# Optimization experiments

Hardware: AMD Instinct MI355X
Metric: run time of the kernel (lower is better)

Reference implementation:

```python
import jax, jax.numpy as jnp
import numpy as np

DMODEL = 1024
N_EXPERTS = 16
EXPERT_SIZE = 256
K = 4


def setup_inputs() -> dict:
    key = jax.random.key(0)
    k1, k2, k3, k4 = jax.random.split(key, 4)
    std_sel = 1.0 / np.sqrt(DMODEL)
    std_val = 1.0 / np.sqrt(N_EXPERTS * EXPERT_SIZE)
    return {
        "x": jax.random.normal(k1, (4, 2048, DMODEL), dtype=jnp.float32),
        "expert_sel": jax.random.normal(k2, (N_EXPERTS, DMODEL), dtype=jnp.float32) * std_sel,
        "keys": jax.random.normal(k3, (N_EXPERTS, DMODEL, EXPERT_SIZE), dtype=jnp.float32) * std_sel,
        "values": jax.random.normal(k4, (N_EXPERTS, EXPERT_SIZE, DMODEL), dtype=jnp.float32) * std_val,
        "route_scale": jnp.ones((1,), dtype=jnp.float32),
    }


def reference(x, expert_sel, keys, values, route_scale):
    # Routing: sigmoid gating, top-k selection (eval mode: no dropout/bias balancing)
    sel_logits = jnp.einsum("btd,ed->bte", x, expert_sel)  # [B,T,E]
    sel_probs = jax.nn.sigmoid(sel_logits)
    _, sel_index = jax.lax.top_k(sel_probs, K)  # [B,T,K]
    sel_val = jnp.take_along_axis(sel_probs, sel_index, axis=-1)  # [B,T,K]
    sel_val = sel_val / jnp.clip(sel_val.sum(-1, keepdims=True), 1e-9)
    sel_val = sel_val * route_scale  # route_scale shape [1] broadcasts
    # Dense all-expert FFN (as in original), then gather top-k and combine
    scores_all = jax.nn.relu(jnp.einsum("btd,edh->bteh", x, keys))  # [B,T,E,H]
    values_all = jnp.einsum("bteh,ehv->btev", scores_all, values)   # [B,T,E,V]
    sel_idx_exp = sel_index[..., None]  # [B,T,K,1]
    selected = jnp.take_along_axis(values_all, sel_idx_exp, axis=2)  # [B,T,K,V]
    out = (selected * sel_val[..., None]).sum(axis=2)  # [B,T,V]
    return out
```

## Files before the change

### kernel.cpp

```cpp
#include <hip/hip_runtime.h>
#include <math.h>


constexpr int NTOK = 8192;
constexpr int DM   = 1024;
constexpr int NE   = 16;
constexpr int EH   = 256;
constexpr int TK   = 4;
constexpr int CAP  = 8192;
constexpr int BM   = 64;

typedef __attribute__((ext_vector_type(8))) short short8;
typedef __attribute__((ext_vector_type(4))) float f32x4;

#define MFMA16(a, b, c) __builtin_amdgcn_mfma_f32_16x16x32_bf16(a, b, c, 0, 0, 0)
#define VMCNT(n) asm volatile("s_waitcnt vmcnt(" #n ")" ::: "memory")
#define SBAR     __builtin_amdgcn_s_barrier()
#define SCHED0   __builtin_amdgcn_sched_barrier(0)

__device__ __forceinline__ void gload_lds16(const void* g, void* l) {
    __builtin_amdgcn_global_load_lds(
        (const __attribute__((address_space(1))) void*)g,
        (__attribute__((address_space(3))) void*)l, 16, 0, 0);
}

__device__ __forceinline__ unsigned short f2bf(float f) {
    union { float f; unsigned int u; } x; x.f = f;
    unsigned int r = x.u + 0x7fffu + ((x.u >> 16) & 1u);
    return (unsigned short)(r >> 16);
}
__device__ __forceinline__ float bf2f(unsigned short b) {
    union { unsigned int u; float f; } x; x.u = ((unsigned int)b) << 16;
    return x.f;
}

__global__ __launch_bounds__(256) void route_conv_kernel(
    const float* __restrict__ x, const float* __restrict__ esel,
    const float* __restrict__ rscale,
    unsigned short* __restrict__ xb,
    int4* __restrict__ sel4, float* __restrict__ wtk)
{
    __shared__ float Es[NE * DM];
    int tid = threadIdx.x;

    {
        const float4* src = (const float4*)esel;
        float4* dst = (float4*)Es;
        #pragma unroll
        for (int j = 0; j < 16; ++j) dst[tid + j * 256] = src[tid + j * 256];
    }
    __syncthreads();

    int t    = blockIdx.x * 8 + (tid >> 5);
    int l32  = tid & 31;

    float acc[NE];
    #pragma unroll
    for (int e = 0; e < NE; ++e) acc[e] = 0.f;

    const float4* x4 = (const float4*)(x + (size_t)t * DM);
    const float4* E4 = (const float4*)Es;
    #pragma unroll
    for (int i4 = 0; i4 < 8; ++i4) {
        int d4 = i4 * 32 + l32;
        float4 xv = x4[d4];
        ushort4 cb = { f2bf(xv.x), f2bf(xv.y), f2bf(xv.z), f2bf(xv.w) };
        *(ushort4*)(xb + (size_t)t * DM + d4 * 4) = cb;
        #pragma unroll
        for (int e = 0; e < NE; ++e) {
            float4 wv = E4[e * 256 + d4];
            acc[e] = fmaf(xv.x, wv.x, acc[e]);
            acc[e] = fmaf(xv.y, wv.y, acc[e]);
            acc[e] = fmaf(xv.z, wv.z, acc[e]);
            acc[e] = fmaf(xv.w, wv.w, acc[e]);
        }
    }

    #pragma unroll
    for (int off = 16; off; off >>= 1)
        #pragma unroll
        for (int e = 0; e < NE; ++e)
            acc[e] += __shfl_xor(acc[e], off, 32);

    if (l32 == 0) {
        float p[NE];
        #pragma unroll
        for (int e = 0; e < NE; ++e) p[e] = 1.0f / (1.0f + expf(-acc[e]));

        int   sel_e[TK];
        float sel_p[TK];
        float sum = 0.f;
        #pragma unroll
        for (int k = 0; k < TK; ++k) {
            float best = -INFINITY; int be = NE;
            #pragma unroll
            for (int e = 0; e < NE; ++e) {
                bool take = p[e] > best;
                best = take ? p[e] : best;
                be   = take ? e    : be;
            }
            sel_e[k] = be; sel_p[k] = best; sum += best;
            #pragma unroll
            for (int e = 0; e < NE; ++e) p[e] = (e == be) ? -INFINITY : p[e];
        }

        float wsc = rscale[0] / fmaxf(sum, 1e-9f);
        int4 s = { sel_e[0], sel_e[1], sel_e[2], sel_e[3] };
        sel4[t] = s;
        float4 wv = { sel_p[0] * wsc, sel_p[1] * wsc,
                      sel_p[2] * wsc, sel_p[3] * wsc };
        *(float4*)(wtk + t * TK) = wv;
    }
}

__global__ __launch_bounds__(1024) void compact_kernel(
    const int4* __restrict__ sel4, int* __restrict__ counts,
    int* __restrict__ lpk)
{
    __shared__ int wsum[16];
    int e    = blockIdx.x;
    int tid  = threadIdx.x;
    int w    = tid >> 6;
    int lane = tid & 63;

    int base = 0;
    for (int c = 0; c < NTOK; c += 1024) {
        int t = c + tid;
        int4 s = sel4[t];
        int k = -1;
        if      (s.x == e) k = 0;
        else if (s.y == e) k = 1;
        else if (s.z == e) k = 2;
        else if (s.w == e) k = 3;
        unsigned long long m = __ballot(k >= 0);
        int rank = __popcll(m & ((1ull << lane) - 1ull));
        if (lane == 63) wsum[w] = __popcll(m);
        __syncthreads();
        int prefix = 0, total = 0;
        #pragma unroll
        for (int i = 0; i < 16; ++i) {
            int v = wsum[i];
            prefix += (i < w) ? v : 0;
            total  += v;
        }
        if (k >= 0) lpk[e * CAP + base + prefix + rank] = t * TK + k;
        base += total;
        __syncthreads();
    }
    if (tid == 0) counts[e] = base;
}

__global__ __launch_bounds__(256) void transF_kernel(
    const float* __restrict__ in, unsigned short* __restrict__ outp, int R, int C)
{
    __shared__ float T[32][33];
    int e = blockIdx.z;
    int r0 = blockIdx.y * 32, c0 = blockIdx.x * 32;
    int ri = threadIdx.x >> 3, cq = threadIdx.x & 7;
    float4 v = *(const float4*)(in + ((size_t)e * R + r0 + ri) * C + c0 + cq * 4);
    T[ri][cq * 4 + 0] = v.x; T[ri][cq * 4 + 1] = v.y;
    T[ri][cq * 4 + 2] = v.z; T[ri][cq * 4 + 3] = v.w;
    __syncthreads();
    int ci = threadIdx.x >> 3, rq = threadIdx.x & 7;
    int row = c0 + ci;
    int kb  = r0 + rq * 4;
    int nk32 = R >> 5;
    size_t chunk = (size_t)e * (C >> 4) * nk32 + (size_t)(row >> 4) * nk32 + (kb >> 5);
    size_t off = chunk * 512 +
                 (size_t)(((((kb >> 3) & 3) * 16 + (row & 15)) * 8) + (kb & 7));
    ushort4 o = { f2bf(T[rq * 4 + 0][ci]), f2bf(T[rq * 4 + 1][ci]),
                  f2bf(T[rq * 4 + 2][ci]), f2bf(T[rq * 4 + 3][ci]) };
    *(ushort4*)(outp + off) = o;
}

template<int USE_SCRATCH>
__global__ __launch_bounds__(256) void ffn_kernel(
    const unsigned short* __restrict__ xb,
    const unsigned short* __restrict__ ktbF,
    const unsigned short* __restrict__ vtbF,
    const int* __restrict__ counts, const int* __restrict__ lpk,
    const float* __restrict__ wtk,
    unsigned short* __restrict__ scratch,
    float* __restrict__ out)
{
    __shared__ __align__(16) char L[12288 + 32768 + 768];
    char* const Xb = L;
    char* const Ss = L + 12288;
    int*   stok = (int*)(L + 45056);
    int*   spk  = (int*)(L + 45056 + 256);
    float* sw   = (float*)(L + 45056 + 512);

    int tid  = threadIdx.x;
    int lane = tid & 63;
    int w    = tid >> 6;
    int lm   = lane & 15;
    int q    = lane >> 4;
    int lane8 = lane * 8;

    int xp = blockIdx.x & 7;
    int j0 = blockIdx.x >> 3;
    int e0 = xp * 2;
    int c0 = counts[e0], c1 = counts[e0 + 1];
    int n0 = (c0 + BM - 1) >> 6;
    int ntot = n0 + ((c1 + BM - 1) >> 6);

    for (int jt = j0; jt < ntot; jt += 64) {
        int e, t0, cnt;
        if (jt < n0) { e = e0;     t0 = jt << 6;        cnt = c0; }
        else         { e = e0 + 1; t0 = (jt - n0) << 6; cnt = c1; }

        if (tid < BM) {
            int s = t0 + tid;
            if (s < cnt) {
                int pk = lpk[e * CAP + s];
                stok[tid] = pk >> 2; spk[tid] = pk; sw[tid] = wtk[pk];
            } else {
                stok[tid] = 0; spk[tid] = USE_SCRATCH ? (NTOK * TK) : 0; sw[tid] = 0.f;
            }
        }
        __syncthreads();

        int rowX = tid >> 2;
        int cb   = ((tid & 3) * 16) ^ (((rowX >> 1) & 3) << 4);
        const unsigned short* srcX = xb + (size_t)stok[rowX] * DM + (cb >> 1);
        const unsigned short* kfe  = ktbF + (size_t)e * 262144;
        const unsigned short* vfe  = vtbF + (size_t)e * 262144;
        int w4  = w * 4;
        int w16 = w * 16;

        auto stageX = [&](int n) {
            if (n < 32)
                gload_lds16(srcX + n * 32, Xb + (n % 3) * 4096 + tid * 16);
        };
        auto loadK = [&](short8 (&kr)[4], int n) {
            if (n < 32) {
                #pragma unroll
                for (int ni = 0; ni < 4; ++ni)
                    kr[ni] = *(const short8*)(kfe + (((w4 + ni) * 32 + n) << 9) + lane8);
            }
        };

        f32x4 zero = {0.f, 0.f, 0.f, 0.f};
        f32x4 acc[4][4];
        #pragma unroll
        for (int mi = 0; mi < 4; ++mi)
            #pragma unroll
            for (int ni = 0; ni < 4; ++ni) acc[mi][ni] = zero;

        short8 krA[4], krB[4];

        stageX(0); stageX(1); loadK(krA, 0);
        SCHED0;
        loadK(krB, 1);
        SCHED0;

        auto step1 = [&](int n, short8 (&kr)[4]) {
            if (n == 0)       { VMCNT(4); }
            else if (n == 31) { VMCNT(0); }
            else              { VMCNT(5); }
            SBAR; SCHED0;
            stageX(n + 2);
            const char* XB = Xb + (n % 3) * 4096;
            short8 a[4];
            #pragma unroll
            for (int mi = 0; mi < 4; ++mi) {
                int row = mi * 16 + lm;
                a[mi] = *(const short8*)(XB + row * 64 +
                         ((q * 16) ^ (((row >> 1) & 3) << 4)));
            }
            __builtin_amdgcn_s_setprio(1);
            #pragma unroll
            for (int mi = 0; mi < 4; ++mi)
                #pragma unroll
                for (int ni = 0; ni < 4; ++ni)
                    acc[mi][ni] = MFMA16(a[mi], kr[ni], acc[mi][ni]);
            __builtin_amdgcn_s_setprio(0);
            loadK(kr, n + 2);
        };

        #pragma unroll
        for (int n = 0; n < 32; ++n) {
            if (n & 1) step1(n, krB);
            else       step1(n, krA);
        }

        int   spk_[4][4];
        float sw_[4][4];
        int   stok_[4][4];
        #pragma unroll
        for (int mi = 0; mi < 4; ++mi)
            #pragma unroll
            for (int r = 0; r < 4; ++r) {
                int slot = mi * 16 + q * 4 + r;
                spk_[mi][r] = spk[slot];
                if (!USE_SCRATCH) { sw_[mi][r] = sw[slot]; stok_[mi][r] = stok[slot]; }
            }

        #pragma unroll
        for (int mi = 0; mi < 4; ++mi)
            #pragma unroll
            for (int ni = 0; ni < 4; ++ni) {
                f32x4 v = acc[mi][ni];
                #pragma unroll
                for (int r = 0; r < 4; ++r) {
                    int row = mi * 16 + q * 4 + r;
                    int col = w * 64 + ni * 16 + lm;
                    *(unsigned short*)(Ss + row * 512 +
                        ((col * 2) ^ ((row & 7) << 4))) = f2bf(fmaxf(v[r], 0.f));
                }
            }
        __syncthreads();

        short8 vA[4], vB[4];
        auto loadV = [&](short8 (&vr)[4], int u) {
            if (u < 32) {
                int d16b = w16 + ((u >> 3) << 2);
                int kk = u & 7;
                #pragma unroll
                for (int ni = 0; ni < 4; ++ni)
                    vr[ni] = *(const short8*)(vfe + ((((size_t)(d16b + ni)) * 8 + kk) << 9) + lane8);
            }
        };
        loadV(vA, 0); loadV(vB, 1);

        f32x4 acc2[4][4];
        auto step2 = [&](int u, short8 (&vr)[4]) {
            int kk = u & 7, nb = u >> 3;
            if (kk == 0) {
                #pragma unroll
                for (int mi = 0; mi < 4; ++mi)
                    #pragma unroll
                    for (int ni = 0; ni < 4; ++ni) acc2[mi][ni] = zero;
            }
            short8 a2[4];
            #pragma unroll
            for (int mi = 0; mi < 4; ++mi) {
                int row = mi * 16 + lm;
                a2[mi] = *(const short8*)(Ss + row * 512 +
                          ((kk * 64 + q * 16) ^ ((row & 7) << 4)));
            }
            __builtin_amdgcn_s_setprio(1);
            #pragma unroll
            for (int mi = 0; mi < 4; ++mi)
                #pragma unroll
                for (int ni = 0; ni < 4; ++ni)
                    acc2[mi][ni] = MFMA16(a2[mi], vr[ni], acc2[mi][ni]);
            __builtin_amdgcn_s_setprio(0);
            loadV(vr, u + 2);
            if (kk == 7) {
                #pragma unroll
                for (int mi = 0; mi < 4; ++mi)
                    #pragma unroll
                    for (int r = 0; r < 4; ++r) {
                        if (USE_SCRATCH) {
                            unsigned int lo = (unsigned int)f2bf(acc2[mi][0][r]) |
                                              ((unsigned int)f2bf(acc2[mi][1][r]) << 16);
                            unsigned int hi = (unsigned int)f2bf(acc2[mi][2][r]) |
                                              ((unsigned int)f2bf(acc2[mi][3][r]) << 16);
                            uint2 pv = { lo, hi };
                            *(uint2*)(scratch + (size_t)spk_[mi][r] * DM +
                                      (w4 + nb) * 64 + lm * 4) = pv;
                        } else {
                            #pragma unroll
                            for (int ni = 0; ni < 4; ++ni) {
                                int d = w * 256 + nb * 64 + ni * 16 + lm;
                                atomicAdd(out + (size_t)stok_[mi][r] * DM + d,
                                          sw_[mi][r] * acc2[mi][ni][r]);
                            }
                        }
                    }
            }
        };

        #pragma unroll
        for (int u = 0; u < 32; ++u) {
            if (u & 1) step2(u, vB);
            else       step2(u, vA);
        }
    }
}

__global__ __launch_bounds__(256) void combine_kernel(
    const unsigned short* __restrict__ scratch, const float* __restrict__ wtk,
    float* __restrict__ out)
{
    int t   = blockIdx.x * 2 + (threadIdx.x >> 7);
    int l   = threadIdx.x & 127;
    int blk = l >> 3;
    int lm2 = l & 7;
    float o[8] = {0.f, 0.f, 0.f, 0.f, 0.f, 0.f, 0.f, 0.f};
    #pragma unroll
    for (int k = 0; k < TK; ++k) {
        float wv = wtk[t * TK + k];
        uint4 qv = *(const uint4*)(scratch + (size_t)(t * TK + k) * DM +
                                   blk * 64 + lm2 * 8);
        unsigned int us[4] = { qv.x, qv.y, qv.z, qv.w };
        #pragma unroll
        for (int j = 0; j < 4; ++j) {
            o[j * 2 + 0] = fmaf(wv, bf2f((unsigned short)(us[j] & 0xffff)), o[j * 2 + 0]);
            o[j * 2 + 1] = fmaf(wv, bf2f((unsigned short)(us[j] >> 16)),    o[j * 2 + 1]);
        }
    }
    float* ob = out + (size_t)t * DM + blk * 64 + 2 * lm2;
    #pragma unroll
    for (int ni = 0; ni < 4; ++ni) {
        float2 f2 = { o[ni], o[ni + 4] };
        *(float2*)(ob + ni * 16) = f2;
    }
}

extern "C" void kernel_launch(void* const* d_in, const int* in_sizes, int n_in,
                              void* d_out, int out_size, void* d_ws, size_t ws_size,
                              hipStream_t stream) {
    const float* x      = (const float*)d_in[0];
    const float* esel   = (const float*)d_in[1];
    const float* keys   = (const float*)d_in[2];
    const float* values = (const float*)d_in[3];
    const float* rscale = (const float*)d_in[4];
    float* out = (float*)d_out;

    char* ws = (char*)d_ws;
    size_t o = 0;
    auto alloc = [&](size_t sz) { size_t r = o; o = (o + sz + 255) & ~(size_t)255; return r; };
    size_t o_counts = alloc(NE * 4);
    size_t o_lpk    = alloc((size_t)NE * CAP * 4);
    size_t o_sel4   = alloc((size_t)NTOK * 16);
    size_t o_wtk    = alloc((size_t)NTOK * TK * 4);
    size_t o_xb     = alloc((size_t)NTOK * DM * 2);
    size_t o_ktb    = alloc((size_t)NE * EH * DM * 2);
    size_t o_vtb    = alloc((size_t)NE * DM * EH * 2);
    size_t o_scr    = alloc(((size_t)NTOK * TK + BM) * DM * 2);
    size_t need_full = o;

    int*            counts  = (int*)(ws + o_counts);
    int*            lpk     = (int*)(ws + o_lpk);
    int4*           sel4    = (int4*)(ws + o_sel4);
    float*          wtk     = (float*)(ws + o_wtk);
    unsigned short* xb      = (unsigned short*)(ws + o_xb);
    unsigned short* ktbF    = (unsigned short*)(ws + o_ktb);
    unsigned short* vtbF    = (unsigned short*)(ws + o_vtb);
    unsigned short* scratch = (unsigned short*)(ws + o_scr);

    bool use_scratch = ws_size >= need_full;

    if (!use_scratch)
        hipMemsetAsync(d_out, 0, (size_t)out_size * sizeof(float), stream);

    route_conv_kernel<<<NTOK / 8, 256, 0, stream>>>(x, esel, rscale, xb,
                                                    sel4, wtk);
    compact_kernel<<<NE, 1024, 0, stream>>>(sel4, counts, lpk);
    transF_kernel<<<dim3(EH / 32, DM / 32, NE), 256, 0, stream>>>(keys, ktbF, DM, EH);
    transF_kernel<<<dim3(DM / 32, EH / 32, NE), 256, 0, stream>>>(values, vtbF, EH, DM);

    if (use_scratch) {
        ffn_kernel<1><<<512, 256, 0, stream>>>(
            xb, ktbF, vtbF, counts, lpk, wtk, scratch, out);
        combine_kernel<<<NTOK / 2, 256, 0, stream>>>(scratch, wtk, out);
    } else {
        ffn_kernel<0><<<512, 256, 0, stream>>>(
            xb, ktbF, vtbF, counts, lpk, wtk, scratch, out);
    }
}
```

Baseline: 138.2 us.

## Load X fragments directly into registers instead of staging through LDS

Phase one of the FFN kernel used to stage gathered token rows of X into a triple-buffered LDS ring with global_load_lds, barriers and explicit vmcnt waits. It now has each wave load its X fragments straight from global memory into registers, double-buffered alongside the K fragments. This removes the per-step barriers and frees 12 KB of LDS, so launch bounds now request 3 blocks per SM. The cost is redundant global reads of X across the four waves, no software-controlled wait scheduling, a partially unrolled phase-two loop, and an extra barrier at the end of each tile.

```diff
diff --git a/kernel.cpp b/kernel.cpp
--- a/kernel.cpp
+++ b/kernel.cpp
@@ -14,15 +14,6 @@
 typedef __attribute__((ext_vector_type(4))) float f32x4;
 
 #define MFMA16(a, b, c) __builtin_amdgcn_mfma_f32_16x16x32_bf16(a, b, c, 0, 0, 0)
-#define VMCNT(n) asm volatile("s_waitcnt vmcnt(" #n ")" ::: "memory")
-#define SBAR     __builtin_amdgcn_s_barrier()
-#define SCHED0   __builtin_amdgcn_sched_barrier(0)
-
-__device__ __forceinline__ void gload_lds16(const void* g, void* l) {
-    __builtin_amdgcn_global_load_lds(
-        (const __attribute__((address_space(1))) void*)g,
-        (__attribute__((address_space(3))) void*)l, 16, 0, 0);
-}
 
 __device__ __forceinline__ unsigned short f2bf(float f) {
     union { float f; unsigned int u; } x; x.f = f;
@@ -174,7 +165,7 @@
 }
 
 template<int USE_SCRATCH>
-__global__ __launch_bounds__(256) void ffn_kernel(
+__global__ __launch_bounds__(256, 3) void ffn_kernel(
     const unsigned short* __restrict__ xb,
     const unsigned short* __restrict__ ktbF,
     const unsigned short* __restrict__ vtbF,
@@ -183,12 +174,11 @@
     unsigned short* __restrict__ scratch,
     float* __restrict__ out)
 {
-    __shared__ __align__(16) char L[12288 + 32768 + 768];
-    char* const Xb = L;
-    char* const Ss = L + 12288;
-    int*   stok = (int*)(L + 45056);
-    int*   spk  = (int*)(L + 45056 + 256);
-    float* sw   = (float*)(L + 45056 + 512);
+    __shared__ __align__(16) char L[32768 + 768];
+    char* const Ss = L;
+    int*   stok = (int*)(L + 32768);
+    int*   spk  = (int*)(L + 32768 + 256);
+    float* sw   = (float*)(L + 32768 + 512);
 
     int tid  = threadIdx.x;
     int lane = tid & 63;
@@ -220,17 +210,22 @@
         }
         __syncthreads();
 
-        int rowX = tid >> 2;
-        int cb   = ((tid & 3) * 16) ^ (((rowX >> 1) & 3) << 4);
-        const unsigned short* srcX = xb + (size_t)stok[rowX] * DM + (cb >> 1);
-        const unsigned short* kfe  = ktbF + (size_t)e * 262144;
-        const unsigned short* vfe  = vtbF + (size_t)e * 262144;
+        const unsigned short* kfe = ktbF + (size_t)e * 262144;
+        const unsigned short* vfe = vtbF + (size_t)e * 262144;
         int w4  = w * 4;
         int w16 = w * 16;
 
-        auto stageX = [&](int n) {
-            if (n < 32)
-                gload_lds16(srcX + n * 32, Xb + (n % 3) * 4096 + tid * 16);
+        const unsigned short* xrow[4];
+        #pragma unroll
+        for (int mi = 0; mi < 4; ++mi)
+            xrow[mi] = xb + (size_t)stok[mi * 16 + lm] * DM + q * 8;
+
+        auto loadX = [&](short8 (&xr)[4], int n) {
+            if (n < 32) {
+                #pragma unroll
+                for (int mi = 0; mi < 4; ++mi)
+                    xr[mi] = *(const short8*)(xrow[mi] + n * 32);
+            }
         };
         auto loadK = [&](short8 (&kr)[4], int n) {
             if (n < 32) {
@@ -247,41 +242,26 @@
             #pragma unroll
             for (int ni = 0; ni < 4; ++ni) acc[mi][ni] = zero;
 
-        short8 krA[4], krB[4];
-
-        stageX(0); stageX(1); loadK(krA, 0);
-        SCHED0;
-        loadK(krB, 1);
-        SCHED0;
-
-        auto step1 = [&](int n, short8 (&kr)[4]) {
-            if (n == 0)       { VMCNT(4); }
-            else if (n == 31) { VMCNT(0); }
-            else              { VMCNT(5); }
-            SBAR; SCHED0;
-            stageX(n + 2);
-            const char* XB = Xb + (n % 3) * 4096;
-            short8 a[4];
-            #pragma unroll
-            for (int mi = 0; mi < 4; ++mi) {
-                int row = mi * 16 + lm;
-                a[mi] = *(const short8*)(XB + row * 64 +
-                         ((q * 16) ^ (((row >> 1) & 3) << 4)));
-            }
+        short8 xA[4], xB[4], kA[4], kB[4];
+        loadX(xA, 0); loadK(kA, 0);
+        loadX(xB, 1); loadK(kB, 1);
+        for (int n = 0; n < 32; n += 2) {
             __builtin_amdgcn_s_setprio(1);
             #pragma unroll
             for (int mi = 0; mi < 4; ++mi)
                 #pragma unroll
                 for (int ni = 0; ni < 4; ++ni)
-                    acc[mi][ni] = MFMA16(a[mi], kr[ni], acc[mi][ni]);
+                    acc[mi][ni] = MFMA16(xA[mi], kA[ni], acc[mi][ni]);
             __builtin_amdgcn_s_setprio(0);
-            loadK(kr, n + 2);
-        };
-
-        #pragma unroll
-        for (int n = 0; n < 32; ++n) {
-            if (n & 1) step1(n, krB);
-            else       step1(n, krA);
+            loadX(xA, n + 2); loadK(kA, n + 2);
+            __builtin_amdgcn_s_setprio(1);
+            #pragma unroll
+            for (int mi = 0; mi < 4; ++mi)
+                #pragma unroll
+                for (int ni = 0; ni < 4; ++ni)
+                    acc[mi][ni] = MFMA16(xB[mi], kB[ni], acc[mi][ni]);
+            __builtin_amdgcn_s_setprio(0);
+            loadX(xB, n + 3); loadK(kB, n + 3);
         }
 
         int   spk_[4][4];
@@ -372,11 +352,12 @@
             }
         };
 
-        #pragma unroll
+        #pragma unroll 2
         for (int u = 0; u < 32; ++u) {
             if (u & 1) step2(u, vB);
             else       step2(u, vA);
         }
+        __syncthreads();
     }
 }
 
```

New measurement: 190.5 us. 37.8% more time.
